# Performance work log

Hardware: AMD Instinct MI355X
Metric: run time of the kernel (lower is better)

Reference implementation:

```python
import jax, jax.numpy as jnp
import numpy as np

N = 50000   # nodes
E = 800000  # edges
G = 64      # graphs in batch
D = 128     # num_input
H = 128     # num_hidden
O = 10      # num_output


def _linear_params(key, fan_in, fan_out):
    k1, k2 = jax.random.split(key)
    s = 1.0 / np.sqrt(fan_in)
    W = jax.random.uniform(k1, (fan_out, fan_in), jnp.float32, -s, s)
    b = jax.random.uniform(k2, (fan_out,), jnp.float32, -s, s)
    return W, b


def setup_inputs() -> dict:
    key = jax.random.key(0)
    ks = jax.random.split(key, 12)
    x = jax.random.normal(ks[0], (N, D), jnp.float32)
    edge_index = jax.random.randint(ks[1], (2, E), 0, N, dtype=jnp.int32).astype(jnp.int64)
    batch = jnp.sort(jax.random.randint(ks[2], (N,), 0, G, dtype=jnp.int32)).astype(jnp.int64)

    W_rel1, b_rel1 = _linear_params(ks[3], D, H)
    W_root1, _ = _linear_params(ks[4], D, H)
    W_rel2, b_rel2 = _linear_params(ks[5], H, H)
    W_root2, _ = _linear_params(ks[6], H, H)
    W_rel3, b_rel3 = _linear_params(ks[7], H, H)
    W_root3, _ = _linear_params(ks[8], H, H)
    W1, b1 = _linear_params(ks[9], 2 * H, 128)
    W2, b2 = _linear_params(ks[10], 128, 64)
    W3, b3 = _linear_params(ks[11], 64, O)

    return dict(x=x, edge_index=edge_index, batch=batch,
                W_rel1=W_rel1, b_rel1=b_rel1, W_root1=W_root1,
                W_rel2=W_rel2, b_rel2=b_rel2, W_root2=W_root2,
                W_rel3=W_rel3, b_rel3=b_rel3, W_root3=W_root3,
                W1=W1, b1=b1, W2=W2, b2=b2, W3=W3, b3=b3)


def _graph_conv(x, src, dst, W_rel, b_rel, W_root):
    # PyG GraphConv (aggr='add'): out_i = W_rel @ sum_{j->i} x_j + b_rel + W_root @ x_i
    agg = jax.ops.segment_sum(x[src], dst, num_segments=N)  # [N, d]
    return agg @ W_rel.T + b_rel + x @ W_root.T


def _pool(x, batch):
    # concat(global_max_pool, global_mean_pool) -> [G, 2d]
    mx = jax.ops.segment_max(x, batch, num_segments=G)
    mx = jnp.where(jnp.isfinite(mx), mx, 0.0)  # guard empty segments
    sm = jax.ops.segment_sum(x, batch, num_segments=G)
    cnt = jax.ops.segment_sum(jnp.ones((x.shape[0], 1), x.dtype), batch, num_segments=G)
    mean = sm / jnp.maximum(cnt, 1.0)
    return jnp.concatenate([mx, mean], axis=1)


def reference(x, edge_index, batch,
              W_rel1, b_rel1, W_root1,
              W_rel2, b_rel2, W_root2,
              W_rel3, b_rel3, W_root3,
              W1, b1, W2, b2, W3, b3):
    src, dst = edge_index[0], edge_index[1]
    h = jax.nn.relu(_graph_conv(x, src, dst, W_rel1, b_rel1, W_root1))
    x1 = _pool(h, batch)
    h = jax.nn.relu(_graph_conv(h, src, dst, W_rel2, b_rel2, W_root2))
    x2 = _pool(h, batch)
    h = jax.nn.relu(_graph_conv(h, src, dst, W_rel3, b_rel3, W_root3))
    x3 = _pool(h, batch)
    node_embs = h
    graph_emb = x1 + x2 + x3           # [G, 2H]
    z = jax.nn.relu(graph_emb @ W1.T + b1)
    z = jax.nn.relu(z @ W2.T + b2)     # dropout p=0 -> no-op
    logits = z @ W3.T + b3             # [G, O]
    return logits, node_embs, graph_emb
```

## Files before the change

kernel.cpp:

```cpp
#include <hip/hip_runtime.h>
#include <hip/hip_bf16.h>

#define NN 50000
#define EE 800000
#define GG 64
#define NBUCK 196
#define ABLOCKS 125
#define CHUNK 6400
#define BCAP 8192
#define SPANCAP 512
#define PARTN 3125

typedef __attribute__((ext_vector_type(8))) short bf16x8;
typedef __attribute__((ext_vector_type(4))) float f32x4;
typedef __attribute__((ext_vector_type(4))) unsigned int u32x4;

__device__ __forceinline__ float bflo(unsigned u) { return __uint_as_float(u << 16); }
__device__ __forceinline__ float bfhi(unsigned u) { return __uint_as_float(u & 0xffff0000u); }
__device__ __forceinline__ float b2f(unsigned short s) { return __uint_as_float(((unsigned)s) << 16); }
__device__ __forceinline__ unsigned short f2bf(float f) {
    __hip_bfloat16 h = __float2bfloat16(f);
    union { __hip_bfloat16 h; unsigned short u; } cv; cv.h = h; return cv.u;
}

__global__ void detect_kernel(const unsigned* __restrict__ xw,
                              const unsigned* __restrict__ eiw,
                              int* __restrict__ flags,
                              int* __restrict__ gstart) {
    __shared__ int s_cnt, s_nz;
    if (threadIdx.x == 0) { s_cnt = 0; s_nz = 0; }
    if (threadIdx.x < 65) gstart[threadIdx.x] = NN;
    __syncthreads();
    int cnt = 0;
    for (int i = threadIdx.x; i < 4096; i += 256) {
        unsigned w = xw[(size_t)i * 711];
        unsigned elo = (w >> 7) & 0xFF;
        if (elo >= 100 && elo <= 140) cnt++;
    }
    int nz = 0;
    for (int i = threadIdx.x; i < 1024; i += 256) {
        unsigned w = eiw[(size_t)i * 1560 + 1];
        if (w != 0) nz++;
    }
    atomicAdd(&s_cnt, cnt);
    atomicAdd(&s_nz, nz);
    __syncthreads();
    if (threadIdx.x == 0) {
        flags[0] = (s_cnt < 3600) ? 1 : 0;
        flags[1] = (s_nz  < 8)    ? 1 : 0;
    }
}

struct WPtrs { const void* p[15]; };

__global__ __launch_bounds__(256) void prep_kernel(const void* __restrict__ xsrc,
                                                   const unsigned* __restrict__ eiw,
                                                   const unsigned* __restrict__ bw,
                                                   WPtrs wp,
                                                   unsigned short* __restrict__ arena,
                                                   int* __restrict__ counts,
                                                   uint4* __restrict__ zero_region,
                                                   int* __restrict__ gstart,
                                                   const int* __restrict__ flags) {
    const int b = blockIdx.x;
    const int tid = threadIdx.x;
    const int isF32 = flags[0];

    if (b < 3125) {
        const int total4 = NN * 128 / 4;
        for (int i = b * 256 + tid; i < total4; i += 800000) {
            uint2 o;
            if (isF32) {
                float4 f = ((const float4*)xsrc)[i];
                o.x = (unsigned)f2bf(f.x) | ((unsigned)f2bf(f.y) << 16);
                o.y = (unsigned)f2bf(f.z) | ((unsigned)f2bf(f.w) << 16);
            } else {
                o = ((const uint2*)xsrc)[i];
            }
            ((uint2*)arena)[i] = o;
        }
    } else if (b < 3674) {
        const int cnt[15] = {16384,128,16384, 16384,128,16384, 16384,128,16384,
                             32768,128,8192,64,640,10};
        const int dst[15] = {19200000,19232768,19216384, 19232896,19265664,19249280,
                             19265792,19298560,19282176,
                             19298688,19331456,19331584,19339776,19339840,19340480};
        const int total = 140490;
        int i = (b - 3125) * 256 + tid;
        if (i < total) {
            int seg = 0, base = 0;
            while (i - base >= cnt[seg]) { base += cnt[seg]; ++seg; }
            int off = i - base;
            const void* s = wp.p[seg];
            arena[dst[seg] + off] =
                isF32 ? f2bf(((const float*)s)[off]) : ((const unsigned short*)s)[off];
        }
    } else if (b < 3799) {
        __shared__ int hist[256];
        hist[tid] = 0;
        __syncthreads();
        const int i64 = flags[1];
        const int e0 = (b - 3674) * CHUNK;
        for (int it = 0; it < CHUNK / 256; ++it) {
            int e = e0 + it * 256 + tid;
            int d = (int)(i64 ? eiw[(size_t)2 * (EE + e)] : eiw[EE + e]);
            atomicAdd(&hist[d >> 8], 1);
        }
        __syncthreads();
        counts[(b - 3674) * 256 + tid] = hist[tid];
    } else if (b < 4055) {
        zero_region[(b - 3799) * 256 + tid] = (uint4){0, 0, 0, 0};
    } else {
        const int i64 = flags[1];
        int i = (b - 4055) * 256 + tid;
        if (i < NN) {
            int g  = (int)(i64 ? bw[(size_t)2 * i] : bw[i]);
            int gp = (i == 0) ? -1 : (int)(i64 ? bw[(size_t)2 * (i - 1)] : bw[i - 1]);
            for (int gg = gp + 1; gg <= g; ++gg) gstart[gg] = i;
        }
    }
}

__global__ __launch_bounds__(256) void bucket_offsets(const int* __restrict__ counts,
                                                      int* __restrict__ offsets,
                                                      int* __restrict__ bucket_base) {
    __shared__ int s[256];
    const int t = threadIdx.x;
    int col = 0;
    for (int b = 0; b < ABLOCKS; ++b) col += counts[b * 256 + t];
    s[t] = col;
    __syncthreads();
    for (int d = 1; d < 256; d <<= 1) {
        int x = (t >= d) ? s[t - d] : 0;
        __syncthreads();
        s[t] += x;
        __syncthreads();
    }
    int base = s[t] - col;
    bucket_base[t] = base;
    if (t == 255) bucket_base[256] = s[255];
    int run = base;
    for (int b = 0; b < ABLOCKS; ++b) {
        offsets[b * 256 + t] = run;
        run += counts[b * 256 + t];
    }
}

__global__ __launch_bounds__(256) void bucket_scatter(const unsigned* __restrict__ eiw,
                                                      const int* __restrict__ offsets,
                                                      unsigned* __restrict__ packed,
                                                      const int* __restrict__ flags) {
    __shared__ int cur[256];
    cur[threadIdx.x] = offsets[blockIdx.x * 256 + threadIdx.x];
    __syncthreads();
    int i64 = flags[1];
    int e0 = blockIdx.x * CHUNK;
    for (int it = 0; it < CHUNK / 256; ++it) {
        int e = e0 + it * 256 + threadIdx.x;
        int s = (int)(i64 ? eiw[(size_t)2 * e]        : eiw[e]);
        int d = (int)(i64 ? eiw[(size_t)2 * (EE + e)] : eiw[EE + e]);
        int pos = atomicAdd(&cur[d >> 8], 1);
        packed[pos] = ((unsigned)s << 8) | (unsigned)(d & 255);
    }
}

__global__ __launch_bounds__(256) void bucket_sort(const unsigned* __restrict__ packed,
                                                   const int* __restrict__ bucket_base,
                                                   unsigned short* __restrict__ csr_src,
                                                   int* __restrict__ row_ptr) {
    __shared__ unsigned sbuf[BCAP];
    __shared__ int hist[256];
    __shared__ int cur[256];
    const int t = threadIdx.x;
    const int b = blockIdx.x;
    const int lo = bucket_base[b];
    int n = bucket_base[b + 1] - lo;
    if (n > BCAP) n = BCAP;

    hist[t] = 0;
    __syncthreads();
    for (int i = t; i < n; i += 256) {
        unsigned p = packed[lo + i];
        sbuf[i] = p;
        atomicAdd(&hist[p & 255], 1);
    }
    __syncthreads();
    int v = hist[t];
    __shared__ int s[256];
    s[t] = v;
    __syncthreads();
    for (int d = 1; d < 256; d <<= 1) {
        int x = (t >= d) ? s[t - d] : 0;
        __syncthreads();
        s[t] += x;
        __syncthreads();
    }
    int start = s[t] - v;
    int node = b * 256 + t;
    if (node < NN) row_ptr[node] = lo + start;
    if (b == 0 && t == 0) row_ptr[NN] = EE;
    cur[t] = start;
    __syncthreads();
    for (int i = t; i < n; i += 256) {
        unsigned p = sbuf[i];
        int pos = atomicAdd(&cur[p & 255], 1);
        csr_src[lo + pos] = (unsigned short)(p >> 8);
    }
}

__global__ __launch_bounds__(256, 4) void conv_fused(const unsigned short* __restrict__ hin,
                                                     const int* __restrict__ row_ptr,
                                                     const unsigned short* __restrict__ csr16,
                                                     const unsigned short* __restrict__ Wrel,
                                                     const unsigned short* __restrict__ Wroot,
                                                     const unsigned short* __restrict__ brel,
                                                     const unsigned* __restrict__ bw,
                                                     unsigned* __restrict__ pmx,
                                                     float* __restrict__ psum,
                                                     unsigned* __restrict__ ppart,
                                                     unsigned short* __restrict__ outb,
                                                     void* __restrict__ outG,
                                                     const int* __restrict__ flags) {
    __shared__ __align__(16) unsigned short tile[16][136];
    __shared__ int sbatch[16];
    __shared__ int s_rp[17];
    __shared__ unsigned short s_idx[SPANCAP];

    const int tid  = threadIdx.x;
    const int wv   = tid >> 6;
    const int lane = tid & 63;
    const int m0   = blockIdx.x * 16;
    const int mrow = lane & 15;
    const int quad = lane >> 4;

    if (tid < 17) s_rp[tid] = row_ptr[m0 + tid];
    if (tid >= 32 && tid < 48) {
        const int i64 = flags[1];
        int rr = m0 + (tid - 32);
        sbatch[tid - 32] = (int)(i64 ? bw[(size_t)2 * rr] : bw[rr]);
    }
    __syncthreads();
    const int base = s_rp[0];
    const int span = s_rp[16] - base;
    const int nst  = (span < SPANCAP) ? span : SPANCAP;
    for (int i = tid; i < nst; i += 256) s_idx[i] = csr16[base + i];

    bf16x8 rootv[4];
    #pragma unroll
    for (int k2 = 0; k2 < 4; ++k2)
        rootv[k2] = *(const bf16x8*)(hin + (size_t)(m0 + mrow) * 128 + k2 * 32 + quad * 8);

    __syncthreads();

    const int qd  = lane >> 4;
    const int l16 = lane & 15;
    const int lr  = wv * 4 + qd;
    const int jb  = s_rp[lr]     - base;
    const int je  = s_rp[lr + 1] - base;
    const uint4* h16 = (const uint4*)hin;

    float a0 = 0.f, a1 = 0.f, a2 = 0.f, a3 = 0.f,
          a4 = 0.f, a5 = 0.f, a6 = 0.f, a7 = 0.f;

    if (span <= SPANCAP) {
        int j = jb;
        for (; j + 16 <= je; j += 16) {
            int idx[16];
            #pragma unroll
            for (int q = 0; q < 16; ++q) idx[q] = s_idx[j + q];
            uint4 u[16];
            #pragma unroll
            for (int q = 0; q < 16; ++q) u[q] = h16[(size_t)idx[q] * 16 + l16];
            #pragma unroll
            for (int q = 0; q < 16; ++q) {
                a0 += bflo(u[q].x); a1 += bfhi(u[q].x);
                a2 += bflo(u[q].y); a3 += bfhi(u[q].y);
                a4 += bflo(u[q].z); a5 += bfhi(u[q].z);
                a6 += bflo(u[q].w); a7 += bfhi(u[q].w);
            }
        }
        if (j + 8 <= je) {
            int idx[8];
            #pragma unroll
            for (int q = 0; q < 8; ++q) idx[q] = s_idx[j + q];
            uint4 u[8];
            #pragma unroll
            for (int q = 0; q < 8; ++q) u[q] = h16[(size_t)idx[q] * 16 + l16];
            #pragma unroll
            for (int q = 0; q < 8; ++q) {
                a0 += bflo(u[q].x); a1 += bfhi(u[q].x);
                a2 += bflo(u[q].y); a3 += bfhi(u[q].y);
                a4 += bflo(u[q].z); a5 += bfhi(u[q].z);
                a6 += bflo(u[q].w); a7 += bfhi(u[q].w);
            }
            j += 8;
        }
        if (j < je) {
            #pragma unroll
            for (int q = 0; q < 8; ++q) {
                int ii = j + q;
                int ic = (ii < je - 1) ? ii : (je - 1);
                float sc = (ii < je) ? 1.f : 0.f;
                uint4 u = h16[(size_t)s_idx[ic] * 16 + l16];
                a0 = fmaf(bflo(u.x), sc, a0); a1 = fmaf(bfhi(u.x), sc, a1);
                a2 = fmaf(bflo(u.y), sc, a2); a3 = fmaf(bfhi(u.y), sc, a3);
                a4 = fmaf(bflo(u.z), sc, a4); a5 = fmaf(bfhi(u.z), sc, a5);
                a6 = fmaf(bflo(u.w), sc, a6); a7 = fmaf(bfhi(u.w), sc, a7);
            }
        }
    } else {
        for (int j = jb; j < je; j += 8) {
            #pragma unroll
            for (int q = 0; q < 8; ++q) {
                int ii = j + q;
                int ic = (ii < je - 1) ? ii : (je - 1);
                float sc = (ii < je) ? 1.f : 0.f;
                uint4 u = h16[(size_t)csr16[base + ic] * 16 + l16];
                a0 = fmaf(bflo(u.x), sc, a0); a1 = fmaf(bfhi(u.x), sc, a1);
                a2 = fmaf(bflo(u.y), sc, a2); a3 = fmaf(bfhi(u.y), sc, a3);
                a4 = fmaf(bflo(u.z), sc, a4); a5 = fmaf(bfhi(u.z), sc, a5);
                a6 = fmaf(bflo(u.w), sc, a6); a7 = fmaf(bfhi(u.w), sc, a7);
            }
        }
    }

    {
        uint4 o;
        o.x = (unsigned)f2bf(a0) | ((unsigned)f2bf(a1) << 16);
        o.y = (unsigned)f2bf(a2) | ((unsigned)f2bf(a3) << 16);
        o.z = (unsigned)f2bf(a4) | ((unsigned)f2bf(a5) << 16);
        o.w = (unsigned)f2bf(a6) | ((unsigned)f2bf(a7) << 16);
        *(uint4*)&tile[lr][l16 * 8] = o;
    }
    __syncthreads();

    f32x4 acc[2];
    acc[0] = (f32x4){0.f, 0.f, 0.f, 0.f};
    acc[1] = (f32x4){0.f, 0.f, 0.f, 0.f};

    #pragma unroll
    for (int kk = 0; kk < 8; ++kk) {
        const unsigned short* Bs = (kk < 4) ? Wrel : Wroot;
        const int kc = (kk & 3) * 32 + quad * 8;
        bf16x8 a;
        if (kk < 4) a = *(const bf16x8*)&tile[mrow][kc];
        else        a = rootv[kk - 4];
        #pragma unroll
        for (int n = 0; n < 2; ++n) {
            const int col0 = (wv * 2 + n) * 16;
            bf16x8 b = *(const bf16x8*)(Bs + (size_t)(col0 + mrow) * 128 + kc);
            acc[n] = __builtin_amdgcn_mfma_f32_16x16x32_bf16(a, b, acc[n], 0, 0, 0);
        }
    }

    __syncthreads();

    #pragma unroll
    for (int n = 0; n < 2; ++n) {
        const int col = (wv * 2 + n) * 16 + mrow;
        const float bias = b2f(brel[col]);
        #pragma unroll
        for (int i = 0; i < 4; ++i) {
            const int lrow = quad * 4 + i;
            float v = fmaxf(acc[n][i] + bias, 0.f);
            tile[lrow][col] = f2bf(v);
        }
    }
    __syncthreads();

    const int isF32 = flags[0];
    {
        const int lr2 = tid >> 4;
        const int c16 = tid & 15;
        u32x4 v = *(const u32x4*)&tile[lr2][c16 * 8];
        __builtin_nontemporal_store(v, (u32x4*)outb + (size_t)(m0 + lr2) * 16 + c16);
        if (outG) {
            if (isF32) {
                f32x4* p = (f32x4*)outG + 160 + (size_t)(m0 + lr2) * 32 + c16 * 2;
                f32x4 f0 = (f32x4){bflo(v.x), bfhi(v.x), bflo(v.y), bfhi(v.y)};
                f32x4 f1 = (f32x4){bflo(v.z), bfhi(v.z), bflo(v.w), bfhi(v.w)};
                __builtin_nontemporal_store(f0, p);
                __builtin_nontemporal_store(f1, p + 1);
            } else {
                u32x4* p = (u32x4*)((unsigned short*)outG + 640);
                __builtin_nontemporal_store(v, p + (size_t)(m0 + lr2) * 16 + c16);
            }
        }
    }

    if (tid < 128) {
        const int col = tid;
        const int slice = blockIdx.x & 7;
        int rr = 0;
        float mx = 0.f, sm = 0.f;
        if (ppart) {
            const int g0 = sbatch[0];
            for (; rr < 16 && sbatch[rr] == g0; ++rr) {
                float v = b2f(tile[rr][col]);
                mx = fmaxf(mx, v); sm += v;
            }
            ppart[(size_t)blockIdx.x * 128 + col] =
                (unsigned)f2bf(mx) | ((unsigned)f2bf(sm) << 16);
            mx = 0.f; sm = 0.f;
        }
        if (rr < 16) {
            int curg = sbatch[rr];
            for (; rr < 16; ++rr) {
                int g = sbatch[rr];
                if (g != curg) {
                    atomicMax(&pmx[(slice * GG + curg) * 128 + col], __float_as_uint(mx));
                    unsafeAtomicAdd(&psum[(slice * GG + curg) * 128 + col], sm);
                    curg = g; mx = 0.f; sm = 0.f;
                }
                float v = b2f(tile[rr][col]);
                mx = fmaxf(mx, v);
                sm += v;
            }
            atomicMax(&pmx[(slice * GG + curg) * 128 + col], __float_as_uint(mx));
            unsafeAtomicAdd(&psum[(slice * GG + curg) * 128 + col], sm);
        }
    }
}

__global__ __launch_bounds__(256) void mlp_kernel(const unsigned* __restrict__ pmxL,
                                                  const float* __restrict__ psum,
                                                  const unsigned* __restrict__ part,
                                                  const int* __restrict__ gstart,
                                                  const unsigned short* __restrict__ W1,
                                                  const unsigned short* __restrict__ b1,
                                                  const unsigned short* __restrict__ W2,
                                                  const unsigned short* __restrict__ b2,
                                                  const unsigned short* __restrict__ W3,
                                                  const unsigned short* __restrict__ b3,
                                                  void* __restrict__ out,
                                                  const int* __restrict__ flags) {
    int g = blockIdx.x;
    int t = threadIdx.x;
    int isF32 = flags[0];
    __shared__ float sge[256];
    __shared__ float sz1[128];
    __shared__ float sz2[64];

    int start = gstart[g];
    int end   = gstart[g + 1];
    int cnt   = end - start;

    int b_lo = (start + 15) >> 4;
    int b_hi = (cnt > 0) ? ((end - 1) >> 4) : (b_lo - 1);

    float v;
    if (t < 128) {
        v = 0.f;
        #pragma unroll
        for (int L = 0; L < 3; ++L) {
            float m = 0.f;
            #pragma unroll
            for (int s = 0; s < 8; ++s)
                m = fmaxf(m, __uint_as_float(pmxL[((L * 8 + s) * GG + g) * 128 + t]));
            if (part) {
                const unsigned* pm = part + (size_t)L * PARTN * 128;
                for (int b = b_lo; b <= b_hi; ++b)
                    m = fmaxf(m, b2f((unsigned short)(pm[(size_t)b * 128 + t] & 0xffffu)));
            }
            v += m;
        }
    } else {
        float sm = 0.f;
        #pragma unroll
        for (int s = 0; s < 8; ++s) sm += psum[(s * GG + g) * 128 + (t - 128)];
        if (part) {
            #pragma unroll
            for (int L = 0; L < 3; ++L) {
                const unsigned* pm = part + (size_t)L * PARTN * 128;
                for (int b = b_lo; b <= b_hi; ++b)
                    sm += b2f((unsigned short)(pm[(size_t)b * 128 + (t - 128)] >> 16));
            }
        }
        v = sm / fmaxf((float)cnt, 1.f);
    }
    sge[t] = v;
    size_t geo = (size_t)640 + (size_t)NN * 128 + (size_t)g * 256 + t;
    if (isF32) ((float*)out)[geo] = v;
    else       ((unsigned short*)out)[geo] = f2bf(v);
    __syncthreads();

    if (t < 128) {
        float acc = b2f(b1[t]);
        for (int k = 0; k < 256; ++k) acc = fmaf(sge[k], b2f(W1[t * 256 + k]), acc);
        sz1[t] = fmaxf(acc, 0.f);
    }
    __syncthreads();
    if (t < 64) {
        float acc = b2f(b2[t]);
        for (int k = 0; k < 128; ++k) acc = fmaf(sz1[k], b2f(W2[t * 128 + k]), acc);
        sz2[t] = fmaxf(acc, 0.f);
    }
    __syncthreads();
    if (t < 10) {
        float acc = b2f(b3[t]);
        for (int k = 0; k < 64; ++k) acc = fmaf(sz2[k], b2f(W3[t * 64 + k]), acc);
        size_t o = (size_t)g * 10 + t;
        if (isF32) ((float*)out)[o] = acc;
        else       ((unsigned short*)out)[o] = f2bf(acc);
    }
}

#define XBF_OFF   0
#define HA_OFF    6400000
#define HB_OFF    12800000
#define WR1_OFF   19200000
#define WO1_OFF   19216384
#define BR1_OFF   19232768
#define WR2_OFF   19232896
#define WO2_OFF   19249280
#define BR2_OFF   19265664
#define WR3_OFF   19265792
#define WO3_OFF   19282176
#define BR3_OFF   19298560
#define W1_OFF    19298688
#define B1_OFF    19331456
#define W2_OFF    19331584
#define B2_OFF    19339776
#define W3_OFF    19339840
#define B3_OFF    19340480
#define ARENA_END 19340490

extern "C" void kernel_launch(void* const* d_in, const int* in_sizes, int n_in,
                              void* d_out, int out_size, void* d_ws, size_t ws_size,
                              hipStream_t stream) {
    unsigned short* arena = (unsigned short*)d_ws;
    size_t intBase = ((size_t)ARENA_END * 2 + 255) & ~(size_t)255;
    char* ib = (char*)d_ws + intBase;
    int*            row_ptr = (int*)ib;
    unsigned short* csr_src = (unsigned short*)(ib + 200064);
    unsigned*       packed  = (unsigned*)(ib + 1800064);
    int*            counts  = (int*)(ib + 5000064);
    int*            offsets = (int*)(ib + 5128064);
    int*            bbase   = (int*)(ib + 5256064);
    unsigned*       part    = (unsigned*)(ib + 1800064);
    unsigned*       pmxL    = (unsigned*)(ib + 6600064);
    float*          psum    = (float*)(ib + 7386496);
    int*            flags   = (int*)(ib + 7648640);
    int*            gstart  = (int*)(ib + 7648768);

    size_t need = intBase + 7649028;
    unsigned* partP = (ws_size >= need) ? part : nullptr;

    const unsigned* eiw = (const unsigned*)d_in[1];
    const unsigned* bw  = (const unsigned*)d_in[2];
    dim3 blk(256);

    detect_kernel<<<1, 256, 0, stream>>>((const unsigned*)d_in[0], eiw, flags, gstart);

    WPtrs wp;
    for (int i = 0; i < 15; ++i) wp.p[i] = d_in[3 + i];
    prep_kernel<<<4251, blk, 0, stream>>>(d_in[0], eiw, bw, wp, arena, counts,
                                          (uint4*)pmxL, gstart, flags);

    bucket_offsets<<<1, blk, 0, stream>>>(counts, offsets, bbase);
    bucket_scatter<<<ABLOCKS, blk, 0, stream>>>(eiw, offsets, packed, flags);
    bucket_sort<<<NBUCK, blk, 0, stream>>>(packed, bbase, csr_src, row_ptr);

    const int convGrid = NN / 16;

    conv_fused<<<convGrid, blk, 0, stream>>>(arena + XBF_OFF, row_ptr, csr_src,
                                             arena + WR1_OFF, arena + WO1_OFF, arena + BR1_OFF,
                                             bw, pmxL, psum,
                                             partP,
                                             arena + HA_OFF, nullptr, flags);
    conv_fused<<<convGrid, blk, 0, stream>>>(arena + HA_OFF, row_ptr, csr_src,
                                             arena + WR2_OFF, arena + WO2_OFF, arena + BR2_OFF,
                                             bw, pmxL + 65536, psum,
                                             partP ? partP + (size_t)PARTN * 128 : nullptr,
                                             arena + HB_OFF, nullptr, flags);
    conv_fused<<<convGrid, blk, 0, stream>>>(arena + HB_OFF, row_ptr, csr_src,
                                             arena + WR3_OFF, arena + WO3_OFF, arena + BR3_OFF,
                                             bw, pmxL + 131072, psum,
                                             partP ? partP + (size_t)2 * PARTN * 128 : nullptr,
                                             arena + XBF_OFF, d_out, flags);

    mlp_kernel<<<GG, blk, 0, stream>>>(pmxL, psum, partP, gstart,
                                       arena + W1_OFF, arena + B1_OFF,
                                       arena + W2_OFF, arena + B2_OFF,
                                       arena + W3_OFF, arena + B3_OFF, d_out, flags);
}
```

Measured before the change: 347.3 us.

## Drop bucket_offsets kernel, infer dtypes on host, fold histogram into prep

Removes the single-block bucket_offsets launch. Per-block histograms are now atomically merged into a global histogram inside prep_kernel, and bucket_scatter and bucket_sort each recompute the prefix scan locally, with a global atomic cursor handing out per-block offsets. Input dtypes are inferred on the host from in_sizes, so the detect kernel can be skipped, along with the bf16 copy of x when the input is already bf16. Output stores become regular instead of nontemporal. The scatter order within a bucket now depends on atomic arrival order, which may change the summation order of edges.

```diff
diff --git a/kernel.cpp b/kernel.cpp
--- a/kernel.cpp
+++ b/kernel.cpp
@@ -23,13 +23,16 @@
     union { __hip_bfloat16 h; unsigned short u; } cv; cv.h = h; return cv.u;
 }
 
+__global__ void init_kernel(int* __restrict__ ghist, int* __restrict__ gcur) {
+    ghist[threadIdx.x] = 0;
+    gcur[threadIdx.x] = 0;
+}
+
 __global__ void detect_kernel(const unsigned* __restrict__ xw,
                               const unsigned* __restrict__ eiw,
-                              int* __restrict__ flags,
-                              int* __restrict__ gstart) {
+                              int* __restrict__ flags) {
     __shared__ int s_cnt, s_nz;
     if (threadIdx.x == 0) { s_cnt = 0; s_nz = 0; }
-    if (threadIdx.x < 65) gstart[threadIdx.x] = NN;
     __syncthreads();
     int cnt = 0;
     for (int i = threadIdx.x; i < 4096; i += 256) {
@@ -59,14 +62,17 @@
                                                    WPtrs wp,
                                                    unsigned short* __restrict__ arena,
                                                    int* __restrict__ counts,
+                                                   int* __restrict__ ghist,
+                                                   int* __restrict__ gstart,
                                                    uint4* __restrict__ zero_region,
-                                                   int* __restrict__ gstart,
+                                                   int hf32, int hi64,
                                                    const int* __restrict__ flags) {
     const int b = blockIdx.x;
     const int tid = threadIdx.x;
-    const int isF32 = flags[0];
 
     if (b < 3125) {
+        if (hf32 == 0) return;
+        const int isF32 = (hf32 > 0) ? 1 : flags[0];
         const int total4 = NN * 128 / 4;
         for (int i = b * 256 + tid; i < total4; i += 800000) {
             uint2 o;
@@ -80,6 +86,7 @@
             ((uint2*)arena)[i] = o;
         }
     } else if (b < 3674) {
+        const int isF32 = (hf32 >= 0) ? hf32 : flags[0];
         const int cnt[15] = {16384,128,16384, 16384,128,16384, 16384,128,16384,
                              32768,128,8192,64,640,10};
         const int dst[15] = {19200000,19232768,19216384, 19232896,19265664,19249280,
@@ -99,7 +106,7 @@
         __shared__ int hist[256];
         hist[tid] = 0;
         __syncthreads();
-        const int i64 = flags[1];
+        const int i64 = (hi64 >= 0) ? hi64 : flags[1];
         const int e0 = (b - 3674) * CHUNK;
         for (int it = 0; it < CHUNK / 256; ++it) {
             int e = e0 + it * 256 + tid;
@@ -108,55 +115,50 @@
         }
         __syncthreads();
         counts[(b - 3674) * 256 + tid] = hist[tid];
-    } else if (b < 4055) {
-        zero_region[(b - 3799) * 256 + tid] = (uint4){0, 0, 0, 0};
-    } else {
-        const int i64 = flags[1];
-        int i = (b - 4055) * 256 + tid;
+        atomicAdd(&ghist[tid], hist[tid]);
+    } else if (b < 3995) {
+        const int i64 = (hi64 >= 0) ? hi64 : flags[1];
+        int i = (b - 3799) * 256 + tid;
         if (i < NN) {
             int g  = (int)(i64 ? bw[(size_t)2 * i] : bw[i]);
             int gp = (i == 0) ? -1 : (int)(i64 ? bw[(size_t)2 * (i - 1)] : bw[i - 1]);
             for (int gg = gp + 1; gg <= g; ++gg) gstart[gg] = i;
-        }
-    }
-}
-
-__global__ __launch_bounds__(256) void bucket_offsets(const int* __restrict__ counts,
-                                                      int* __restrict__ offsets,
-                                                      int* __restrict__ bucket_base) {
-    __shared__ int s[256];
+            if (i == NN - 1)
+                for (int gg = g + 1; gg <= GG; ++gg) gstart[gg] = NN;
+        }
+    } else {
+        zero_region[(b - 3995) * 256 + tid] = (uint4){0, 0, 0, 0};
+    }
+}
+
+__global__ __launch_bounds__(256) void bucket_scatter(const unsigned* __restrict__ eiw,
+                                                      const int* __restrict__ counts,
+                                                      const int* __restrict__ ghist,
+                                                      int* __restrict__ gcur,
+                                                      unsigned* __restrict__ packed,
+                                                      int hi64,
+                                                      const int* __restrict__ flags) {
+    __shared__ int stmp[256];
+    __shared__ int cur[256];
     const int t = threadIdx.x;
-    int col = 0;
-    for (int b = 0; b < ABLOCKS; ++b) col += counts[b * 256 + t];
-    s[t] = col;
+    int gv = ghist[t];
+    stmp[t] = gv;
     __syncthreads();
     for (int d = 1; d < 256; d <<= 1) {
-        int x = (t >= d) ? s[t - d] : 0;
-        __syncthreads();
-        s[t] += x;
-        __syncthreads();
-    }
-    int base = s[t] - col;
-    bucket_base[t] = base;
-    if (t == 255) bucket_base[256] = s[255];
-    int run = base;
-    for (int b = 0; b < ABLOCKS; ++b) {
-        offsets[b * 256 + t] = run;
-        run += counts[b * 256 + t];
-    }
-}
-
-__global__ __launch_bounds__(256) void bucket_scatter(const unsigned* __restrict__ eiw,
-                                                      const int* __restrict__ offsets,
-                                                      unsigned* __restrict__ packed,
-                                                      const int* __restrict__ flags) {
-    __shared__ int cur[256];
-    cur[threadIdx.x] = offsets[blockIdx.x * 256 + threadIdx.x];
-    __syncthreads();
-    int i64 = flags[1];
+        int x = (t >= d) ? stmp[t - d] : 0;
+        __syncthreads();
+        stmp[t] += x;
+        __syncthreads();
+    }
+    int cnt = counts[blockIdx.x * 256 + t];
+    int rel = atomicAdd(&gcur[t], cnt);
+    cur[t] = (stmp[t] - gv) + rel;
+    __syncthreads();
+
+    const int i64 = (hi64 >= 0) ? hi64 : flags[1];
     int e0 = blockIdx.x * CHUNK;
     for (int it = 0; it < CHUNK / 256; ++it) {
-        int e = e0 + it * 256 + threadIdx.x;
+        int e = e0 + it * 256 + t;
         int s = (int)(i64 ? eiw[(size_t)2 * e]        : eiw[e]);
         int d = (int)(i64 ? eiw[(size_t)2 * (EE + e)] : eiw[EE + e]);
         int pos = atomicAdd(&cur[d >> 8], 1);
@@ -165,17 +167,29 @@
 }
 
 __global__ __launch_bounds__(256) void bucket_sort(const unsigned* __restrict__ packed,
-                                                   const int* __restrict__ bucket_base,
+                                                   const int* __restrict__ ghist,
                                                    unsigned short* __restrict__ csr_src,
                                                    int* __restrict__ row_ptr) {
     __shared__ unsigned sbuf[BCAP];
     __shared__ int hist[256];
     __shared__ int cur[256];
+    __shared__ int sg[256];
+    __shared__ int s[256];
     const int t = threadIdx.x;
     const int b = blockIdx.x;
-    const int lo = bucket_base[b];
-    int n = bucket_base[b + 1] - lo;
-    if (n > BCAP) n = BCAP;
+
+    int gv = ghist[t];
+    sg[t] = gv;
+    __syncthreads();
+    for (int d = 1; d < 256; d <<= 1) {
+        int x = (t >= d) ? sg[t - d] : 0;
+        __syncthreads();
+        sg[t] += x;
+        __syncthreads();
+    }
+    const int nb = ghist[b];
+    const int lo = sg[b] - nb;
+    int n = (nb > BCAP) ? BCAP : nb;
 
     hist[t] = 0;
     __syncthreads();
@@ -186,7 +200,6 @@
     }
     __syncthreads();
     int v = hist[t];
-    __shared__ int s[256];
     s[t] = v;
     __syncthreads();
     for (int d = 1; d < 256; d <<= 1) {
@@ -220,6 +233,7 @@
                                                      unsigned* __restrict__ ppart,
                                                      unsigned short* __restrict__ outb,
                                                      void* __restrict__ outG,
+                                                     int hf32, int hi64,
                                                      const int* __restrict__ flags) {
     __shared__ __align__(16) unsigned short tile[16][136];
     __shared__ int sbatch[16];
@@ -235,7 +249,7 @@
 
     if (tid < 17) s_rp[tid] = row_ptr[m0 + tid];
     if (tid >= 32 && tid < 48) {
-        const int i64 = flags[1];
+        const int i64 = (hi64 >= 0) ? hi64 : flags[1];
         int rr = m0 + (tid - 32);
         sbatch[tid - 32] = (int)(i64 ? bw[(size_t)2 * rr] : bw[rr]);
     }
@@ -368,12 +382,12 @@
     }
     __syncthreads();
 
-    const int isF32 = flags[0];
+    const int isF32 = (hf32 >= 0) ? hf32 : flags[0];
     {
         const int lr2 = tid >> 4;
         const int c16 = tid & 15;
         u32x4 v = *(const u32x4*)&tile[lr2][c16 * 8];
-        __builtin_nontemporal_store(v, (u32x4*)outb + (size_t)(m0 + lr2) * 16 + c16);
+        *((u32x4*)outb + (size_t)(m0 + lr2) * 16 + c16) = v;
         if (outG) {
             if (isF32) {
                 f32x4* p = (f32x4*)outG + 160 + (size_t)(m0 + lr2) * 32 + c16 * 2;
@@ -433,10 +447,11 @@
                                                   const unsigned short* __restrict__ W3,
                                                   const unsigned short* __restrict__ b3,
                                                   void* __restrict__ out,
+                                                  int hf32,
                                                   const int* __restrict__ flags) {
     int g = blockIdx.x;
     int t = threadIdx.x;
-    int isF32 = flags[0];
+    int isF32 = (hf32 >= 0) ? hf32 : flags[0];
     __shared__ float sge[256];
     __shared__ float sz1[128];
     __shared__ float sz2[64];
@@ -535,52 +550,68 @@
     unsigned short* csr_src = (unsigned short*)(ib + 200064);
     unsigned*       packed  = (unsigned*)(ib + 1800064);
     int*            counts  = (int*)(ib + 5000064);
-    int*            offsets = (int*)(ib + 5128064);
-    int*            bbase   = (int*)(ib + 5256064);
     unsigned*       part    = (unsigned*)(ib + 1800064);
     unsigned*       pmxL    = (unsigned*)(ib + 6600064);
     float*          psum    = (float*)(ib + 7386496);
-    int*            flags   = (int*)(ib + 7648640);
-    int*            gstart  = (int*)(ib + 7648768);
-
-    size_t need = intBase + 7649028;
+    int*            ghist   = (int*)(ib + 7648640);
+    int*            gcur    = (int*)(ib + 7649664);
+    int*            flags   = (int*)(ib + 7650688);
+    int*            gstart  = (int*)(ib + 7650816);
+
+    size_t need = intBase + 7651076;
     unsigned* partP = (ws_size >= need) ? part : nullptr;
+
+    int hf32 = -1, hi64 = -1;
+    if (in_sizes && n_in >= 2) {
+        if (in_sizes[0] == 25600000)      hf32 = 1;
+        else if (in_sizes[0] == 12800000) hf32 = 0;
+        if (in_sizes[1] == 12800000)      hi64 = 1;
+        else if (in_sizes[1] == 6400000)  hi64 = 0;
+    }
 
     const unsigned* eiw = (const unsigned*)d_in[1];
     const unsigned* bw  = (const unsigned*)d_in[2];
     dim3 blk(256);
 
-    detect_kernel<<<1, 256, 0, stream>>>((const unsigned*)d_in[0], eiw, flags, gstart);
+    init_kernel<<<1, 256, 0, stream>>>(ghist, gcur);
+
+    if (hf32 < 0 || hi64 < 0)
+        detect_kernel<<<1, 256, 0, stream>>>((const unsigned*)d_in[0], eiw, flags);
 
     WPtrs wp;
     for (int i = 0; i < 15; ++i) wp.p[i] = d_in[3 + i];
     prep_kernel<<<4251, blk, 0, stream>>>(d_in[0], eiw, bw, wp, arena, counts,
-                                          (uint4*)pmxL, gstart, flags);
-
-    bucket_offsets<<<1, blk, 0, stream>>>(counts, offsets, bbase);
-    bucket_scatter<<<ABLOCKS, blk, 0, stream>>>(eiw, offsets, packed, flags);
-    bucket_sort<<<NBUCK, blk, 0, stream>>>(packed, bbase, csr_src, row_ptr);
+                                          ghist, gstart, (uint4*)pmxL,
+                                          hf32, hi64, flags);
+
+    bucket_scatter<<<ABLOCKS, blk, 0, stream>>>(eiw, counts, ghist, gcur, packed,
+                                                hi64, flags);
+    bucket_sort<<<NBUCK, blk, 0, stream>>>(packed, ghist, csr_src, row_ptr);
 
     const int convGrid = NN / 16;
 
-    conv_fused<<<convGrid, blk, 0, stream>>>(arena + XBF_OFF, row_ptr, csr_src,
+    const unsigned short* hin1 =
+        (hf32 == 0) ? (const unsigned short*)d_in[0] : (arena + XBF_OFF);
+
+    conv_fused<<<convGrid, blk, 0, stream>>>(hin1, row_ptr, csr_src,
                                              arena + WR1_OFF, arena + WO1_OFF, arena + BR1_OFF,
                                              bw, pmxL, psum,
                                              partP,
-                                             arena + HA_OFF, nullptr, flags);
+                                             arena + HA_OFF, nullptr, hf32, hi64, flags);
     conv_fused<<<convGrid, blk, 0, stream>>>(arena + HA_OFF, row_ptr, csr_src,
                                              arena + WR2_OFF, arena + WO2_OFF, arena + BR2_OFF,
                                              bw, pmxL + 65536, psum,
                                              partP ? partP + (size_t)PARTN * 128 : nullptr,
-                                             arena + HB_OFF, nullptr, flags);
+                                             arena + HB_OFF, nullptr, hf32, hi64, flags);
     conv_fused<<<convGrid, blk, 0, stream>>>(arena + HB_OFF, row_ptr, csr_src,
                                              arena + WR3_OFF, arena + WO3_OFF, arena + BR3_OFF,
                                              bw, pmxL + 131072, psum,
                                              partP ? partP + (size_t)2 * PARTN * 128 : nullptr,
-                                             arena + XBF_OFF, d_out, flags);
+                                             arena + XBF_OFF, d_out, hf32, hi64, flags);
 
     mlp_kernel<<<GG, blk, 0, stream>>>(pmxL, psum, partP, gstart,
                                        arena + W1_OFF, arena + B1_OFF,
                                        arena + W2_OFF, arena + B2_OFF,
-                                       arena + W3_OFF, arena + B3_OFF, d_out, flags);
-}
+                                       arena + W3_OFF, arena + B3_OFF, d_out,
+                                       hf32, flags);
+}
```

Result: faster. 337.8 us (-2.7%).
